# Kernel optimization log

Measured on AMD Instinct MI355X. Metric: run time of the kernel, lower is better.

Reference implementation:

```python
import jax, jax.numpy as jnp
import numpy as np

N_NODES = 100000
N_EDGES = 3200000
N_GRAPHS = 128
F_IN, HID = 16, 64


def setup_inputs() -> dict:
    key = jax.random.key(0)
    ks = jax.random.split(key, 16)
    def lin(k, fan_in, fan_out):
        bound = 1.0 / np.sqrt(fan_in)
        kw, kb = jax.random.split(k)
        W = jax.random.uniform(kw, (fan_in, fan_out), jnp.float32, -bound, bound)
        b = jax.random.uniform(kb, (fan_out,), jnp.float32, -bound, bound)
        return W, b
    x = jax.random.normal(ks[0], (N_NODES, F_IN), jnp.float32)
    edge_index = jax.random.randint(ks[1], (2, N_EDGES), 0, N_NODES, jnp.int64 if jax.config.jax_enable_x64 else jnp.int32)
    edge_attr = jax.random.normal(ks[2], (N_EDGES, 4), jnp.float32)
    batch = jnp.sort(jax.random.randint(ks[3], (N_NODES,), 0, N_GRAPHS))
    W1, b1 = lin(ks[4], F_IN, HID)
    W2, b2 = lin(ks[5], HID, HID)
    W3, b3 = lin(ks[6], HID, HID)
    Wf1, bf1 = lin(ks[7], HID, 32)
    Wf2, bf2 = lin(ks[8], 32, 1)
    return dict(x=x, edge_index=edge_index, edge_attr=edge_attr, batch=batch,
                W1=W1, b1=b1, W2=W2, b2=b2, W3=W3, b3=b3,
                Wf1=Wf1, bf1=bf1, Wf2=Wf2, bf2=bf2)


def _gcn_conv(x, src, dst, norm, W, b, n_nodes):
    # PyG GCNConv: out = scatter_add(norm * (x @ W)[src] -> dst) + b
    h = x @ W                                   # [N, out]
    msg = h[src] * norm[:, None]                # [E+N, out] gather + scale
    agg = jax.ops.segment_sum(msg, dst, num_segments=n_nodes)
    return agg + b


def reference(x, edge_index, edge_attr, batch, W1, b1, W2, b2, W3, b3, Wf1, bf1, Wf2, bf2):
    n = x.shape[0]
    # add self loops (GCNConv default)
    loop = jnp.arange(n, dtype=edge_index.dtype)
    src = jnp.concatenate([edge_index[0], loop])
    dst = jnp.concatenate([edge_index[1], loop])
    # symmetric degree normalization: deg computed on dst with self loops
    deg = jax.ops.segment_sum(jnp.ones_like(src, dtype=x.dtype), dst, num_segments=n)
    dinv = jax.lax.rsqrt(jnp.maximum(deg, 1.0))
    norm = dinv[src] * dinv[dst]

    h = jax.nn.relu(_gcn_conv(x, src, dst, norm, W1, b1, n))   # dropout = identity (eval)
    h = jax.nn.relu(_gcn_conv(h, src, dst, norm, W2, b2, n))
    h = jax.nn.relu(_gcn_conv(h, src, dst, norm, W3, b3, n))

    # global mean pool over graphs
    sums = jax.ops.segment_sum(h, batch, num_segments=N_GRAPHS)          # [B, HID]
    cnts = jax.ops.segment_sum(jnp.ones((n,), x.dtype), batch, num_segments=N_GRAPHS)
    pooled = sums / jnp.maximum(cnts, 1.0)[:, None]

    z = jax.nn.relu(pooled @ Wf1 + bf1)
    return z @ Wf2 + bf2                                                  # [B, 1]
```

## Files before the change

kernel.cpp:

```cpp
#include <hip/hip_runtime.h>
#include <hip/hip_bf16.h>

#define HID 64
#define MAXNB 2048
#define NBLK 512
#define FILL_T 1024
#define HREP 4
#define SEG_CAP 2560

__device__ __forceinline__ float bf2f(unsigned short u) {
    return __uint_as_float(((unsigned)u) << 16);
}
__device__ __forceinline__ unsigned short f2bf(float f) {
    __hip_bfloat16 b = __float2bfloat16(f);
    return *(unsigned short*)&b;
}
__device__ __forceinline__ unsigned packbf(float lo, float hi) {
    return (unsigned)f2bf(lo) | ((unsigned)f2bf(hi) << 16);
}

__global__ __launch_bounds__(FILL_T) void radix_fill2_kernel(
    const int* __restrict__ ei, int* __restrict__ gcur,
    unsigned* __restrict__ ebuf, int E, int NB, int C) {
    __shared__ int lh[HREP * (MAXNB + 1)];
    __shared__ int lcur[MAXNB];
    int blk = blockIdx.x, tid = threadIdx.x;
    for (int i = tid; i < HREP * (MAXNB + 1); i += FILL_T) lh[i] = 0;
    __syncthreads();
    int* lhr = lh + ((tid >> 6) & (HREP - 1)) * (MAXNB + 1);
    int lo = blk * C, hi = min(lo + C, E);
    int cnt = hi - lo;
    int n4 = ((E & 3) == 0) ? (cnt >> 2) : 0;
    const int4* d4 = (const int4*)(ei + (long long)E + lo);
    for (int k = tid; k < n4; k += FILL_T) {
        int4 d = d4[k];
        atomicAdd(&lhr[d.x >> 6], 1);
        atomicAdd(&lhr[d.y >> 6], 1);
        atomicAdd(&lhr[d.z >> 6], 1);
        atomicAdd(&lhr[d.w >> 6], 1);
    }
    for (int e = lo + (n4 << 2) + tid; e < hi; e += FILL_T)
        atomicAdd(&lhr[ei[(long long)E + e] >> 6], 1);
    __syncthreads();
    for (int i = tid; i < NB; i += FILL_T) {
        int v = 0;
#pragma unroll
        for (int r = 0; r < HREP; r++) v += lh[r * (MAXNB + 1) + i];
        int start = v ? atomicAdd(&gcur[i], v) : 0;
        lcur[i] = i * SEG_CAP + start;
    }
    __syncthreads();
    const int4* s4 = (const int4*)(ei + lo);
    for (int k = tid; k < n4; k += FILL_T) {
        int4 s = s4[k];
        int4 d = d4[k];
        int p0 = atomicAdd(&lcur[d.x >> 6], 1);
        int p1 = atomicAdd(&lcur[d.y >> 6], 1);
        int p2 = atomicAdd(&lcur[d.z >> 6], 1);
        int p3 = atomicAdd(&lcur[d.w >> 6], 1);
        ebuf[p0] = ((unsigned)s.x << 6) | (unsigned)(d.x & 63);
        ebuf[p1] = ((unsigned)s.y << 6) | (unsigned)(d.y & 63);
        ebuf[p2] = ((unsigned)s.z << 6) | (unsigned)(d.z & 63);
        ebuf[p3] = ((unsigned)s.w << 6) | (unsigned)(d.w & 63);
    }
    for (int e = lo + (n4 << 2) + tid; e < hi; e += FILL_T) {
        int s = ei[e];
        int d = ei[(long long)E + e];
        int pos = atomicAdd(&lcur[d >> 6], 1);
        ebuf[pos] = ((unsigned)s << 6) | (unsigned)(d & 63);
    }
}

__global__ __launch_bounds__(256) void node_csr_xs_kernel(
    const int* __restrict__ gcur, const unsigned* __restrict__ ebuf,
    const float* __restrict__ x,
    int* __restrict__ row_ptr, int* __restrict__ rend,
    int* __restrict__ col, float* __restrict__ dinv,
    unsigned short* __restrict__ xs, float* __restrict__ sums, int N, int NB) {
    __shared__ unsigned sE[SEG_CAP];
    __shared__ int lcnt[64];
    __shared__ int lcur[64];
    __shared__ float sDv[64];
    int bkt = blockIdx.x, tid = threadIdx.x;
    if (bkt == 0) {
        for (int i = tid; i < 128 * HID; i += 256) sums[i] = 0.f;
    }
    int beg = bkt * SEG_CAP;
    int cnt = min(gcur[bkt], SEG_CAP);
    if (tid < 64) lcnt[tid] = 0;
    for (int i = tid; i < cnt; i += 256) sE[i] = ebuf[beg + i];
    __syncthreads();
    for (int i = tid; i < cnt; i += 256) atomicAdd(&lcnt[sE[i] & 63u], 1);
    __syncthreads();
    if (tid < 64) {
        int v = lcnt[tid];
        int p = v;
#pragma unroll
        for (int off = 1; off < 64; off <<= 1) {
            int t = __shfl_up(p, off);
            if (tid >= off) p += t;
        }
        int base = beg + p - v;
        lcur[tid] = base;
        int node = (bkt << 6) + tid;
        float dv = rsqrtf((float)(v + 1));
        sDv[tid] = dv;
        if (node < N) {
            row_ptr[node] = base;
            rend[node] = base + v;
            dinv[node] = dv;
        }
    }
    __syncthreads();
    for (int i = tid; i < cnt; i += 256) {
        unsigned ev = sE[i];
        int pos = atomicAdd(&lcur[ev & 63u], 1);
        col[pos] = (int)(ev >> 6);
    }
    {
        int r = tid >> 2, q = tid & 3;
        int node = (bkt << 6) + r;
        if (node < N) {
            float dv = sDv[r];
            float4 xv = *(const float4*)(x + (long long)node * 16 + q * 4);
            uint2 w;
            w.x = packbf(dv * xv.x, dv * xv.y);
            w.y = packbf(dv * xv.z, dv * xv.w);
            *(uint2*)(xs + (long long)node * 16 + q * 4) = w;
        }
    }
}

__device__ __forceinline__ void add4(float* acc, uint2 r) {
    acc[0] += __uint_as_float(r.x << 16);
    acc[1] += __uint_as_float(r.x & 0xffff0000u);
    acc[2] += __uint_as_float(r.y << 16);
    acc[3] += __uint_as_float(r.y & 0xffff0000u);
}

__global__ __launch_bounds__(256) void gather16_gemm_kernel(
    const int* __restrict__ row_ptr, const int* __restrict__ rend,
    const int* __restrict__ col,
    const unsigned short* __restrict__ xs,
    const float* __restrict__ W1, const float* __restrict__ b1,
    const float* __restrict__ W2,
    const float* __restrict__ dinv, unsigned short* __restrict__ g2, int N) {
    __shared__ float sW1[16 * HID];
    __shared__ float sW2[HID * HID];
    __shared__ float sB1[HID];
    int tid = threadIdx.x;
    for (int i = tid; i < 16 * HID; i += 256) sW1[i] = W1[i];
    for (int i = tid; i < HID * HID; i += 256) sW2[i] = W2[i];
    if (tid < HID) sB1[tid] = b1[tid];
    __syncthreads();

    int wv = __builtin_amdgcn_readfirstlane(threadIdx.x >> 6);
    int node = blockIdx.x * 4 + wv;
    int lane = threadIdx.x & 63;
    if (node >= N) return;
    int grp = lane >> 2;
    int c = lane & 3;
    int beg = row_ptr[node], end = rend[node];

    float acc[4] = {0.f, 0.f, 0.f, 0.f};
    if (grp == 0) {
        uint2 rs = *(const uint2*)(xs + ((long long)node << 4) + (c << 2));
        add4(acc, rs);
    }
    for (int base = beg; base < end; base += 32) {
        int e0 = base + grp;
        int e1 = e0 + 16;
        bool k0 = e0 < end, k1 = e1 < end;
        int c0 = k0 ? col[e0] : 0;
        int c1 = k1 ? col[e1] : 0;
        uint2 r0 = *(const uint2*)(xs + (((long long)c0) << 4) + (c << 2));
        uint2 r1 = *(const uint2*)(xs + (((long long)c1) << 4) + (c << 2));
        if (k0) add4(acc, r0);
        if (k1) add4(acc, r1);
    }
#pragma unroll
    for (int m = 4; m <= 32; m <<= 1) {
#pragma unroll
        for (int k = 0; k < 4; k++) acc[k] += __shfl_xor(acc[k], m);
    }
    float dv = dinv[node];
    float s1 = 0.f;
#pragma unroll
    for (int f = 0; f < 16; f++) {
        float af = __shfl(acc[f & 3], f >> 2);
        s1 += af * sW1[f * HID + lane];
    }
    float h1 = dv * s1 + sB1[lane];
    h1 = h1 > 0.f ? h1 : 0.f;
    float s2 = 0.f;
#pragma unroll
    for (int k = 0; k < HID; k++) {
        float hk = __shfl(h1, k);
        s2 += hk * sW2[k * HID + lane];
    }
    g2[(long long)node * HID + lane] = f2bf(dv * s2);
}

__device__ __forceinline__ void add8(float* acc, uint4 r) {
    acc[0] += __uint_as_float(r.x << 16);
    acc[1] += __uint_as_float(r.x & 0xffff0000u);
    acc[2] += __uint_as_float(r.y << 16);
    acc[3] += __uint_as_float(r.y & 0xffff0000u);
    acc[4] += __uint_as_float(r.z << 16);
    acc[5] += __uint_as_float(r.z & 0xffff0000u);
    acc[6] += __uint_as_float(r.w << 16);
    acc[7] += __uint_as_float(r.w & 0xffff0000u);
}

__global__ __launch_bounds__(256) void gather_gemm_kernel(
    const int* __restrict__ row_ptr, const int* __restrict__ rend,
    const int* __restrict__ col,
    const unsigned short* __restrict__ g, const float* __restrict__ dinv,
    const float* __restrict__ bias, const float* __restrict__ W3,
    unsigned short* __restrict__ out, int N) {
    __shared__ float sW3[HID * HID];
    __shared__ float sB[HID];
    int tid = threadIdx.x;
    for (int i = tid; i < HID * HID; i += 256) sW3[i] = W3[i];
    if (tid < HID) sB[tid] = bias[tid];
    __syncthreads();

    int wv = __builtin_amdgcn_readfirstlane(threadIdx.x >> 6);
    int node = blockIdx.x * 4 + wv;
    int lane = threadIdx.x & 63;
    if (node >= N) return;
    int grp = lane >> 3;
    int c = lane & 7;
    int beg = row_ptr[node], end = rend[node];

    float acc[8] = {0.f, 0.f, 0.f, 0.f, 0.f, 0.f, 0.f, 0.f};
    if (grp == 0) {
        uint4 rs = *(const uint4*)(g + ((long long)node << 6) + (c << 3));
        add8(acc, rs);
    }
    for (int base = beg; base < end; base += 32) {
        int e0 = base + grp;
        int e1 = e0 + 8, e2 = e0 + 16, e3 = e0 + 24;
        bool k0 = e0 < end, k1 = e1 < end, k2 = e2 < end, k3 = e3 < end;
        int c0 = k0 ? col[e0] : 0;
        int c1 = k1 ? col[e1] : 0;
        int c2 = k2 ? col[e2] : 0;
        int c3 = k3 ? col[e3] : 0;
        uint4 r0 = *(const uint4*)(g + (((long long)c0) << 6) + (c << 3));
        uint4 r1 = *(const uint4*)(g + (((long long)c1) << 6) + (c << 3));
        uint4 r2 = *(const uint4*)(g + (((long long)c2) << 6) + (c << 3));
        uint4 r3 = *(const uint4*)(g + (((long long)c3) << 6) + (c << 3));
        if (k0) add8(acc, r0);
        if (k1) add8(acc, r1);
        if (k2) add8(acc, r2);
        if (k3) add8(acc, r3);
    }
#pragma unroll
    for (int m = 8; m <= 32; m <<= 1) {
#pragma unroll
        for (int k = 0; k < 8; k++) acc[k] += __shfl_xor(acc[k], m);
    }
    float dv = dinv[node];
    float g3 = 0.f;
#pragma unroll
    for (int f = 0; f < HID; f++) {
        float raw = __shfl(acc[f & 7], f >> 3);
        float h2 = dv * raw + sB[f];
        h2 = h2 > 0.f ? h2 : 0.f;
        g3 += h2 * sW3[f * HID + lane];
    }
    out[(long long)node * HID + lane] = f2bf(dv * g3);
}

__global__ __launch_bounds__(256) void gather_kernel(
    const int* __restrict__ row_ptr, const int* __restrict__ rend,
    const int* __restrict__ col,
    const unsigned short* __restrict__ g, const float* __restrict__ dinv,
    const float* __restrict__ bias, unsigned short* __restrict__ h, int N) {
    int wv = __builtin_amdgcn_readfirstlane(threadIdx.x >> 6);
    int node = blockIdx.x * 4 + wv;
    int lane = threadIdx.x & 63;
    if (node >= N) return;
    int grp = lane >> 3;
    int c = lane & 7;
    int beg = row_ptr[node], end = rend[node];

    float acc[8] = {0.f, 0.f, 0.f, 0.f, 0.f, 0.f, 0.f, 0.f};
    if (grp == 0) {
        uint4 rs = *(const uint4*)(g + ((long long)node << 6) + (c << 3));
        add8(acc, rs);
    }
    for (int base = beg; base < end; base += 32) {
        int e0 = base + grp;
        int e1 = e0 + 8, e2 = e0 + 16, e3 = e0 + 24;
        bool k0 = e0 < end, k1 = e1 < end, k2 = e2 < end, k3 = e3 < end;
        int c0 = k0 ? col[e0] : 0;
        int c1 = k1 ? col[e1] : 0;
        int c2 = k2 ? col[e2] : 0;
        int c3 = k3 ? col[e3] : 0;
        uint4 r0 = *(const uint4*)(g + (((long long)c0) << 6) + (c << 3));
        uint4 r1 = *(const uint4*)(g + (((long long)c1) << 6) + (c << 3));
        uint4 r2 = *(const uint4*)(g + (((long long)c2) << 6) + (c << 3));
        uint4 r3 = *(const uint4*)(g + (((long long)c3) << 6) + (c << 3));
        if (k0) add8(acc, r0);
        if (k1) add8(acc, r1);
        if (k2) add8(acc, r2);
        if (k3) add8(acc, r3);
    }
#pragma unroll
    for (int m = 8; m <= 32; m <<= 1) {
#pragma unroll
        for (int k = 0; k < 8; k++) acc[k] += __shfl_xor(acc[k], m);
    }
    if (lane < 8) {
        float dv = dinv[node];
        float4 ba = *(const float4*)(bias + (lane << 3));
        float4 bb = *(const float4*)(bias + (lane << 3) + 4);
        float v0 = dv * acc[0] + ba.x;
        float v1 = dv * acc[1] + ba.y;
        float v2 = dv * acc[2] + ba.z;
        float v3 = dv * acc[3] + ba.w;
        float v4 = dv * acc[4] + bb.x;
        float v5 = dv * acc[5] + bb.y;
        float v6 = dv * acc[6] + bb.z;
        float v7 = dv * acc[7] + bb.w;
        v0 = v0 > 0.f ? v0 : 0.f;
        v1 = v1 > 0.f ? v1 : 0.f;
        v2 = v2 > 0.f ? v2 : 0.f;
        v3 = v3 > 0.f ? v3 : 0.f;
        v4 = v4 > 0.f ? v4 : 0.f;
        v5 = v5 > 0.f ? v5 : 0.f;
        v6 = v6 > 0.f ? v6 : 0.f;
        v7 = v7 > 0.f ? v7 : 0.f;
        uint4 w;
        w.x = (unsigned)f2bf(v0) | ((unsigned)f2bf(v1) << 16);
        w.y = (unsigned)f2bf(v2) | ((unsigned)f2bf(v3) << 16);
        w.z = (unsigned)f2bf(v4) | ((unsigned)f2bf(v5) << 16);
        w.w = (unsigned)f2bf(v6) | ((unsigned)f2bf(v7) << 16);
        *(uint4*)(h + ((long long)node << 6) + (lane << 3)) = w;
    }
}

__global__ void pool_kernel(const unsigned short* __restrict__ h, const int* __restrict__ batch,
                            float* __restrict__ sums, int N) {
    int wave = blockIdx.x * 4 + (threadIdx.x >> 6);
    int lane = threadIdx.x & 63;
    int lo = wave * 16;
    if (lo >= N) return;
    int hi = min(lo + 16, N);
    int curb = batch[lo];
    float sum = 0.f;
    for (int i = lo; i < hi; i++) {
        int b = batch[i];
        if (b != curb) {
            atomicAdd(&sums[curb * HID + lane], sum);
            curb = b; sum = 0.f;
        }
        sum += bf2f(h[(long long)i * HID + lane]);
    }
    atomicAdd(&sums[curb * HID + lane], sum);
}

__global__ void final_kernel(const float* __restrict__ sums, const int* __restrict__ batch,
                             const float* __restrict__ Wf1, const float* __restrict__ bf1,
                             const float* __restrict__ Wf2, const float* __restrict__ bf2,
                             float* __restrict__ out, int N) {
    __shared__ float sW1[HID * 32];
    __shared__ float sW2[32];
    __shared__ int sUB[128];
    int tid = threadIdx.x;
    for (int idx = tid; idx < HID * 32; idx += 128) sW1[idx] = Wf1[idx];
    if (tid < 32) sW2[tid] = Wf2[tid];
    {
        int lo = 0, hi = N;
        while (lo < hi) {
            int mid = (lo + hi) >> 1;
            if (batch[mid] <= tid) lo = mid + 1; else hi = mid;
        }
        sUB[tid] = lo;
    }
    __syncthreads();
    int b = tid;
    float c = (float)(sUB[b] - (b ? sUB[b - 1] : 0));
    c = fmaxf(c, 1.0f);
    float pooled[HID];
#pragma unroll
    for (int j = 0; j < HID; j++) pooled[j] = sums[b * HID + j] / c;
    float o = bf2[0];
#pragma unroll 4
    for (int hd = 0; hd < 32; hd++) {
        float z = bf1[hd];
#pragma unroll
        for (int j = 0; j < HID; j++) z += pooled[j] * sW1[j * 32 + hd];
        z = fmaxf(z, 0.f);
        o += z * sW2[hd];
    }
    out[b] = o;
}

extern "C" void kernel_launch(void* const* d_in, const int* in_sizes, int n_in,
                              void* d_out, int out_size, void* d_ws, size_t ws_size,
                              hipStream_t stream) {
    const float* x     = (const float*)d_in[0];
    const int*   ei    = (const int*)d_in[1];
    const int*   batch = (const int*)d_in[3];
    const float* W1  = (const float*)d_in[4];
    const float* b1  = (const float*)d_in[5];
    const float* W2  = (const float*)d_in[6];
    const float* b2  = (const float*)d_in[7];
    const float* W3  = (const float*)d_in[8];
    const float* b3  = (const float*)d_in[9];
    const float* Wf1 = (const float*)d_in[10];
    const float* bf1 = (const float*)d_in[11];
    const float* Wf2 = (const float*)d_in[12];
    const float* bf2 = (const float*)d_in[13];
    float* out = (float*)d_out;

    const int N  = in_sizes[0] / 16;
    const int E  = in_sizes[1] / 2;
    const int NB = (N + 63) / 64;

    char* ws = (char*)d_ws;
    size_t o = 0;
    float*          dinv    = (float*)(ws + o);          o += ((size_t)N * 4 + 4095) / 4096 * 4096;
    int*            row_ptr = (int*)(ws + o);            o += ((size_t)N * 4 + 4095) / 4096 * 4096;
    int*            rend    = (int*)(ws + o);            o += ((size_t)N * 4 + 4095) / 4096 * 4096;
    int*            gcur    = (int*)(ws + o);            o += ((size_t)NB * 4 + 4095) / 4096 * 4096;
    unsigned*       ebuf    = (unsigned*)(ws + o);       o += (size_t)NB * SEG_CAP * 4;
    int*            col     = (int*)(ws + o);            o += (size_t)NB * SEG_CAP * 4;
    unsigned short* A       = (unsigned short*)(ws + o); o += (size_t)N * HID * 2;
    unsigned short* B       = (unsigned short*)(ws + o); o += (size_t)N * HID * 2;
    unsigned short* XS      = (unsigned short*)(ws + o); o += ((size_t)N * 16 * 2 + 4095) / 4096 * 4096;
    float*          sums    = (float*)(ws + o);          o += 128 * HID * 4;
    (void)ws_size;

    const int T = 256;
    const int Cchunk = (((E + NBLK - 1) / NBLK) + 3) & ~3;
    const int gGa = (N + 3) / 4;
    const int gPool = ((N + 15) / 16 + 3) / 4;

    hipMemsetAsync(gcur, 0, (size_t)NB * 4, stream);
    radix_fill2_kernel<<<NBLK, FILL_T, 0, stream>>>(ei, gcur, ebuf, E, NB, Cchunk);
    node_csr_xs_kernel<<<NB, T, 0, stream>>>(gcur, ebuf, x, row_ptr, rend, col, dinv, XS, sums, N, NB);

    gather16_gemm_kernel<<<gGa, T, 0, stream>>>(row_ptr, rend, col, XS, W1, b1, W2, dinv, A, N);

    gather_gemm_kernel<<<gGa, T, 0, stream>>>(row_ptr, rend, col, A, dinv, b2, W3, B, N);

    gather_kernel<<<gGa, T, 0, stream>>>(row_ptr, rend, col, B, dinv, b3, A, N);

    pool_kernel<<<gPool, T, 0, stream>>>(A, batch, sums, N);
    final_kernel<<<1, 128, 0, stream>>>(sums, batch, Wf1, bf1, Wf2, bf2, out, N);
}
```

Before: 567.0 us.

## Split layer-1 gather from dense GEMM into separate kernels

The fused first-layer kernel, which gathered 16-wide features and then ran two small GEMMs per wavefront, is split in two. A lightweight gather kernel now writes fp32 aggregates to a new workspace buffer, and a separate GEMM kernel processes 16 nodes per block with weights staged in shared memory. The aim is to stop every gather block from loading about 20KB of weights into LDS and running shuffle-heavy per-node GEMMs, which limits occupancy and latency hiding during the irregular gather. In exchange it adds an extra launch and a round trip of the N×16 fp32 intermediate through global memory.

```diff
diff --git a/kernel.cpp b/kernel.cpp
--- a/kernel.cpp
+++ b/kernel.cpp
@@ -138,22 +138,10 @@
     acc[3] += __uint_as_float(r.y & 0xffff0000u);
 }
 
-__global__ __launch_bounds__(256) void gather16_gemm_kernel(
+__global__ __launch_bounds__(256) void gather16_kernel(
     const int* __restrict__ row_ptr, const int* __restrict__ rend,
     const int* __restrict__ col,
-    const unsigned short* __restrict__ xs,
-    const float* __restrict__ W1, const float* __restrict__ b1,
-    const float* __restrict__ W2,
-    const float* __restrict__ dinv, unsigned short* __restrict__ g2, int N) {
-    __shared__ float sW1[16 * HID];
-    __shared__ float sW2[HID * HID];
-    __shared__ float sB1[HID];
-    int tid = threadIdx.x;
-    for (int i = tid; i < 16 * HID; i += 256) sW1[i] = W1[i];
-    for (int i = tid; i < HID * HID; i += 256) sW2[i] = W2[i];
-    if (tid < HID) sB1[tid] = b1[tid];
-    __syncthreads();
-
+    const unsigned short* __restrict__ xs, float* __restrict__ agg, int N) {
     int wv = __builtin_amdgcn_readfirstlane(threadIdx.x >> 6);
     int node = blockIdx.x * 4 + wv;
     int lane = threadIdx.x & 63;
@@ -183,22 +171,60 @@
 #pragma unroll
         for (int k = 0; k < 4; k++) acc[k] += __shfl_xor(acc[k], m);
     }
-    float dv = dinv[node];
-    float s1 = 0.f;
-#pragma unroll
-    for (int f = 0; f < 16; f++) {
-        float af = __shfl(acc[f & 3], f >> 2);
-        s1 += af * sW1[f * HID + lane];
-    }
-    float h1 = dv * s1 + sB1[lane];
-    h1 = h1 > 0.f ? h1 : 0.f;
-    float s2 = 0.f;
-#pragma unroll
-    for (int k = 0; k < HID; k++) {
-        float hk = __shfl(h1, k);
-        s2 += hk * sW2[k * HID + lane];
-    }
-    g2[(long long)node * HID + lane] = f2bf(dv * s2);
+    if (lane < 4) {
+        float4 w = make_float4(acc[0], acc[1], acc[2], acc[3]);
+        *(float4*)(agg + ((long long)node << 4) + (lane << 2)) = w;
+    }
+}
+
+__global__ __launch_bounds__(256) void gemm_agg2_kernel(
+    const float* __restrict__ agg,
+    const float* __restrict__ W1, const float* __restrict__ b1,
+    const float* __restrict__ W2,
+    const float* __restrict__ dinv, unsigned short* __restrict__ g2, int N) {
+    __shared__ float sW1[16 * HID];
+    __shared__ float sW2[HID * HID];
+    __shared__ float sIn[16 * 16];
+    __shared__ float sH[16 * HID];
+    __shared__ float sB1[HID];
+    __shared__ float sDv[16];
+    int tid = threadIdx.x;
+    for (int i = tid; i < 16 * HID; i += 256) sW1[i] = W1[i];
+    for (int i = tid; i < HID * HID; i += 256) sW2[i] = W2[i];
+    if (tid < HID) sB1[tid] = b1[tid];
+    int base = blockIdx.x * 16;
+    {
+        int r = tid >> 4, c = tid & 15;
+        int node = base + r;
+        sIn[tid] = (node < N) ? agg[(long long)node * 16 + c] : 0.f;
+    }
+    if (tid < 16) {
+        int node = base + tid;
+        sDv[tid] = (node < N) ? dinv[node] : 0.f;
+    }
+    __syncthreads();
+    int j = tid & 63;
+    int si = tid >> 6;
+#pragma unroll
+    for (int u = 0; u < 4; u++) {
+        int r = si * 4 + u;
+        float acc = 0.f;
+#pragma unroll
+        for (int k = 0; k < 16; k++) acc += sIn[r * 16 + k] * sW1[k * HID + j];
+        float v = sDv[r] * acc + sB1[j];
+        sH[r * HID + j] = v > 0.f ? v : 0.f;
+    }
+    __syncthreads();
+#pragma unroll
+    for (int u = 0; u < 4; u++) {
+        int r = si * 4 + u;
+        int node = base + r;
+        if (node >= N) continue;
+        float acc = 0.f;
+#pragma unroll 16
+        for (int k = 0; k < HID; k++) acc += sH[r * HID + k] * sW2[k * HID + j];
+        g2[(long long)node * HID + j] = f2bf(sDv[r] * acc);
+    }
 }
 
 __device__ __forceinline__ void add8(float* acc, uint4 r) {
@@ -431,11 +457,13 @@
     unsigned short* A       = (unsigned short*)(ws + o); o += (size_t)N * HID * 2;
     unsigned short* B       = (unsigned short*)(ws + o); o += (size_t)N * HID * 2;
     unsigned short* XS      = (unsigned short*)(ws + o); o += ((size_t)N * 16 * 2 + 4095) / 4096 * 4096;
+    float*          AGG     = (float*)(ws + o);          o += ((size_t)N * 16 * 4 + 4095) / 4096 * 4096;
     float*          sums    = (float*)(ws + o);          o += 128 * HID * 4;
     (void)ws_size;
 
     const int T = 256;
     const int Cchunk = (((E + NBLK - 1) / NBLK) + 3) & ~3;
+    const int gGm = (N + 15) / 16;
     const int gGa = (N + 3) / 4;
     const int gPool = ((N + 15) / 16 + 3) / 4;
 
@@ -443,7 +471,8 @@
     radix_fill2_kernel<<<NBLK, FILL_T, 0, stream>>>(ei, gcur, ebuf, E, NB, Cchunk);
     node_csr_xs_kernel<<<NB, T, 0, stream>>>(gcur, ebuf, x, row_ptr, rend, col, dinv, XS, sums, N, NB);
 
-    gather16_gemm_kernel<<<gGa, T, 0, stream>>>(row_ptr, rend, col, XS, W1, b1, W2, dinv, A, N);
+    gather16_kernel<<<gGa, T, 0, stream>>>(row_ptr, rend, col, XS, AGG, N);
+    gemm_agg2_kernel<<<gGm, T, 0, stream>>>(AGG, W1, b1, W2, dinv, A, N);
 
     gather_gemm_kernel<<<gGa, T, 0, stream>>>(row_ptr, rend, col, A, dinv, b2, W3, B, N);
 
```

New measurement: 508.9 us. 1.11x faster.
